# Performance work log

Measured on AMD Instinct MI355X. Metric: run time of the kernel, lower is better.

The kernel has to match this reference:

```python
import jax, jax.numpy as jnp
import numpy as np

DEGREE = 8
D = 512
K = 256
O = 512
N = 65536


def setup_inputs() -> dict:
    key = jax.random.key(0)
    ks = jax.random.split(key, 4)
    z = jax.random.normal(ks[0], (N, D), dtype=jnp.float32)
    T0 = jnp.ones((K,), dtype=jnp.float32)
    # T[i-1] corresponds to parameter T_i, i = 1..DEGREE, each [K, D]
    T = jax.random.normal(ks[1], (DEGREE, K, D), dtype=jnp.float32) * 0.02
    C_w = jax.random.normal(ks[2], (O, K), dtype=jnp.float32) * (1.0 / np.sqrt(K))
    C_b = jnp.zeros((O,), dtype=jnp.float32)
    return {"z": z, "T0": T0, "T": T, "C_w": C_w, "C_b": C_b}


def reference(z, T0, T, C_w, C_b):
    # z: [N, D]; T: [DEGREE, K, D]; recurrence over polynomial degree n:
    #   out_n = (z @ ((2n-1)/n * T_n).T) * out_{n-1} - (n-1)/n * out_{n-2}
    z = z.reshape(-1, D)
    out_prev2 = T0                                  # degree 0, [K] (broadcasts over N)
    out_prev1 = jnp.einsum('nd,kd->nk', z, T[0])    # degree 1, [N, K]
    for n in range(2, DEGREE + 1):
        a = (2.0 * n - 1.0) / n
        b = (n - 1.0) / n
        cur = jnp.einsum('nd,kd->nk', z, a * T[n - 1]) * out_prev1 - b * out_prev2
        out_prev2, out_prev1 = out_prev1, cur
    # layer_C applied to out_list[degree]
    return out_prev1 @ C_w.T + C_b
```

## Files before the change

### kernel.cpp

```cpp
#include <hip/hip_runtime.h>
#include <hip/hip_fp16.h>
#include <cstdint>

#define NROWS 65536
#define DIM   512
#define KDIM  256
#define ODIM  512
#define DEG   8
#define ZN    (NROWS * DIM)
#define TN    (DEG * KDIM * DIM)
#define CWN   (ODIM * KDIM)

typedef _Float16 f16x8 __attribute__((ext_vector_type(8)));
typedef float    f32x4 __attribute__((ext_vector_type(4)));


__device__ __forceinline__ void gld_lds16(const void* g, void* l) {
  __builtin_amdgcn_global_load_lds(
      (const __attribute__((address_space(1))) unsigned int*)g,
      (__attribute__((address_space(3))) unsigned int*)l, 16, 0, 0);
}

__device__ __forceinline__ unsigned pack2h(float a, float b) {
  union { _Float16 h[2]; unsigned u; } x;
  x.h[0] = (_Float16)a; x.h[1] = (_Float16)b;
  return x.u;
}

__device__ __forceinline__ int swz(int row, int chunk) {
  return (row << 7) | (((chunk + row) & 7) << 4);
}


__global__ void k_convert(const float* __restrict__ z,
                          const float* __restrict__ T,
                          const float* __restrict__ Cw,
                          _Float16* __restrict__ z16,
                          _Float16* __restrict__ Tb,
                          _Float16* __restrict__ Cwb) {
  long e = ((long)blockIdx.x * 256 + threadIdx.x) * 8;
  const float* src;
  _Float16* dst;
  float s = 1.0f;
  if (e < ZN) {
    src = z + e; dst = z16 + e;
  } else {
    long o = e - ZN;
    if (o < TN) {
      int n = (int)(o >> 17);
      s = (n == 0) ? 1.0f : (float)(2 * n + 1) / (float)(n + 1);
      src = T + o; dst = Tb + o;
    } else {
      long c = o - TN;
      if (c >= CWN) return;
      src = Cw + c; dst = Cwb + c;
    }
  }
  float4 v0 = *(const float4*)src;
  float4 v1 = *(const float4*)(src + 4);
  uint4 p;
  p.x = pack2h(v0.x * s, v0.y * s); p.y = pack2h(v0.z * s, v0.w * s);
  p.z = pack2h(v1.x * s, v1.y * s); p.w = pack2h(v1.z * s, v1.w * s);
  *(uint4*)dst = p;
}


__launch_bounds__(256, 3)
__global__ void k_poly(const _Float16* __restrict__ z16,
                       const float* __restrict__ T0,
                       const _Float16* __restrict__ Tb,
                       _Float16* __restrict__ u8) {
  __shared__ __align__(16) uint16_t As[128 * 64];
  __shared__ __align__(16) uint16_t Bs[2][128 * 64];

  const int tid = threadIdx.x;
  const int wave = tid >> 6, lane = tid & 63;

  const int id = blockIdx.x;
  const int super = id >> 8, rem = id & 255;
  const int kg = rem >> 4;
  const int rt = (super << 4) | (rem & 15);
  const int r0 = rt << 7;
  const int k0 = kg << 4;

  const int m_l = lane & 15, kq = lane >> 4;
  const int wrow = wave << 5;

  f32x4 acc[DEG][2];
#pragma unroll
  for (int n = 0; n < DEG; n++)
#pragma unroll
    for (int a = 0; a < 2; a++)
      acc[n][a] = (f32x4){0.f, 0.f, 0.f, 0.f};

  const _Float16* aptr[4];
  const _Float16* bptr[4];
  int lofs[4];
#pragma unroll
  for (int j = 0; j < 4; j++) {
    int lin = (j << 8) + tid;
    int row = lin >> 3;
    int c = ((lin & 7) - row) & 7;
    lofs[j] = lin << 4;
    aptr[j] = z16 + (size_t)(r0 + row) * DIM + (c << 3);
    int n = row >> 4, kk = row & 15;
    bptr[j] = Tb + (size_t)((n << 8) + k0 + kk) * DIM + (c << 3);
  }

  uint4 aR[2][4];

#pragma unroll
  for (int j = 0; j < 4; j++)
    aR[0][j] = *reinterpret_cast<const uint4*>(aptr[j]);
  __builtin_amdgcn_sched_barrier(0);
#pragma unroll
  for (int j = 0; j < 4; j++) gld_lds16(bptr[j], (char*)Bs[0] + lofs[j]);
  __builtin_amdgcn_sched_barrier(0);
#pragma unroll
  for (int j = 0; j < 4; j++)
    aR[1][j] = *reinterpret_cast<const uint4*>(aptr[j] + 64);
  __builtin_amdgcn_sched_barrier(0);

#pragma unroll
  for (int it = 0; it < DIM / 64; it++) {
    const int cur = it & 1;
    __builtin_amdgcn_s_barrier();
    if (it < DIM / 64 - 1)
      asm volatile("s_waitcnt vmcnt(4)" ::: "memory");
    else
      asm volatile("s_waitcnt vmcnt(0)" ::: "memory");
    __builtin_amdgcn_sched_barrier(0);

#pragma unroll
    for (int j = 0; j < 4; j++)
      *(uint4*)((char*)As + lofs[j]) = aR[cur][j];
    __builtin_amdgcn_sched_barrier(0);

    if (it + 1 < DIM / 64) {
#pragma unroll
      for (int j = 0; j < 4; j++)
        gld_lds16(bptr[j] + ((it + 1) << 6), (char*)Bs[cur ^ 1] + lofs[j]);
    }
    __builtin_amdgcn_sched_barrier(0);

    if (it + 2 < DIM / 64) {
#pragma unroll
      for (int j = 0; j < 4; j++)
        aR[cur][j] = *reinterpret_cast<const uint4*>(aptr[j] + ((it + 2) << 6));
    }
    __builtin_amdgcn_sched_barrier(0);

    asm volatile("s_waitcnt lgkmcnt(0)" ::: "memory");
    __builtin_amdgcn_sched_barrier(0);
    __builtin_amdgcn_s_barrier();
    __builtin_amdgcn_sched_barrier(0);

#pragma unroll
    for (int ks = 0; ks < 2; ks++) {
      const int chunk = (ks << 2) + kq;
      f16x8 af[2];
#pragma unroll
      for (int mf = 0; mf < 2; mf++)
        af[mf] = *(const f16x8*)((char*)As + swz(wrow + (mf << 4) + m_l, chunk));
#pragma unroll
      for (int n = 0; n < DEG; n++) {
        f16x8 bv = *(const f16x8*)((char*)Bs[cur] + swz((n << 4) + m_l, chunk));
#pragma unroll
        for (int mf = 0; mf < 2; mf++)
          acc[n][mf] = __builtin_amdgcn_mfma_f32_16x16x32_f16(
              af[mf], bv, acc[n][mf], 0, 0, 0);
      }
    }
  }

  const float bcoef[7] = {1.f/2.f, 2.f/3.f, 3.f/4.f, 4.f/5.f,
                          5.f/6.f, 6.f/7.f, 7.f/8.f};
  const int col = k0 + m_l;
  const float t0v = T0[col];
#pragma unroll
  for (int mf = 0; mf < 2; mf++) {
    f32x4 up2 = {t0v, t0v, t0v, t0v};
    f32x4 up1 = acc[0][mf];
#pragma unroll
    for (int n = 2; n <= DEG; n++) {
      f32x4 cur = acc[n - 1][mf] * up1 - bcoef[n - 2] * up2;
      up2 = up1; up1 = cur;
    }
    const int rbase = r0 + wrow + (mf << 4) + (kq << 2);
#pragma unroll
    for (int r = 0; r < 4; r++)
      u8[(size_t)(rbase + r) * KDIM + col] = (_Float16)up1[r];
  }
}


__launch_bounds__(256, 3)
__global__ void k_out(const _Float16* __restrict__ u8,
                      const _Float16* __restrict__ Cwb,
                      const float* __restrict__ Cb,
                      float* __restrict__ out) {
  __shared__ __align__(16) uint16_t As[2][128 * 64];
  __shared__ __align__(16) uint16_t Bs[2][64 * 64];

  const int tid = threadIdx.x;
  const int wave = tid >> 6, lane = tid & 63;

  const int id = blockIdx.x;
  const int xcd = id & 7;
  const int s = id >> 3;
  const int cg = s & 7;
  const int rt = (xcd << 6) | (s >> 3);
  const int r0 = rt << 7;
  const int c0 = cg << 6;

  const int m_l = lane & 15, kq = lane >> 4;
  const int wrow = wave << 5;

  f32x4 acc[2][4];
#pragma unroll
  for (int a = 0; a < 2; a++)
#pragma unroll
    for (int b = 0; b < 4; b++)
      acc[a][b] = (f32x4){0.f, 0.f, 0.f, 0.f};

  const _Float16* aptr[4];
  const _Float16* bptr[2];
  int lofsA[4], lofsB[2];
#pragma unroll
  for (int j = 0; j < 4; j++) {
    int lin = (j << 8) + tid;
    int row = lin >> 3;
    int c = ((lin & 7) - row) & 7;
    lofsA[j] = lin << 4;
    aptr[j] = u8 + (size_t)(r0 + row) * KDIM + (c << 3);
  }
#pragma unroll
  for (int j = 0; j < 2; j++) {
    int lin = (j << 8) + tid;
    int row = lin >> 3;
    int c = ((lin & 7) - row) & 7;
    lofsB[j] = lin << 4;
    bptr[j] = Cwb + (size_t)(c0 + row) * KDIM + (c << 3);
  }

#pragma unroll
  for (int j = 0; j < 4; j++) gld_lds16(aptr[j], (char*)As[0] + lofsA[j]);
  __builtin_amdgcn_sched_barrier(0);
#pragma unroll
  for (int j = 0; j < 2; j++) gld_lds16(bptr[j], (char*)Bs[0] + lofsB[j]);
  __builtin_amdgcn_sched_barrier(0);

#pragma unroll
  for (int it = 0; it < KDIM / 64; it++) {
    const int cur = it & 1;
    __builtin_amdgcn_s_barrier();
    __builtin_amdgcn_sched_barrier(0);

    if (it + 1 < KDIM / 64) {
#pragma unroll
      for (int j = 0; j < 4; j++)
        gld_lds16(aptr[j] + ((it + 1) << 6), (char*)As[cur ^ 1] + lofsA[j]);
      __builtin_amdgcn_sched_barrier(0);
#pragma unroll
      for (int j = 0; j < 2; j++)
        gld_lds16(bptr[j] + ((it + 1) << 6), (char*)Bs[cur ^ 1] + lofsB[j]);
      __builtin_amdgcn_sched_barrier(0);
      asm volatile("s_waitcnt vmcnt(6)" ::: "memory");
    } else {
      asm volatile("s_waitcnt vmcnt(0)" ::: "memory");
    }
    __builtin_amdgcn_sched_barrier(0);
    __builtin_amdgcn_s_barrier();
    __builtin_amdgcn_sched_barrier(0);

#pragma unroll
    for (int ks = 0; ks < 2; ks++) {
      const int chunk = (ks << 2) + kq;
      f16x8 af[2];
#pragma unroll
      for (int mf = 0; mf < 2; mf++)
        af[mf] = *(const f16x8*)((char*)As[cur] + swz(wrow + (mf << 4) + m_l, chunk));
#pragma unroll
      for (int kf = 0; kf < 4; kf++) {
        f16x8 bv = *(const f16x8*)((char*)Bs[cur] + swz((kf << 4) + m_l, chunk));
#pragma unroll
        for (int mf = 0; mf < 2; mf++)
          acc[mf][kf] = __builtin_amdgcn_mfma_f32_16x16x32_f16(
              af[mf], bv, acc[mf][kf], 0, 0, 0);
      }
    }
  }

#pragma unroll
  for (int kf = 0; kf < 4; kf++) {
    const int col = c0 + (kf << 4) + m_l;
    const float cb = Cb[col];
#pragma unroll
    for (int mf = 0; mf < 2; mf++) {
      const int rbase = r0 + wrow + (mf << 4) + (kq << 2);
#pragma unroll
      for (int r = 0; r < 4; r++)
        out[(size_t)(rbase + r) * ODIM + col] = acc[mf][kf][r] + cb;
    }
  }
}


extern "C" void kernel_launch(void* const* d_in, const int* in_sizes, int n_in,
                              void* d_out, int out_size, void* d_ws, size_t ws_size,
                              hipStream_t stream) {
  const float* z  = (const float*)d_in[0];
  const float* T0 = (const float*)d_in[1];
  const float* T  = (const float*)d_in[2];
  const float* Cw = (const float*)d_in[3];
  const float* Cb = (const float*)d_in[4];
  float* out = (float*)d_out;

  char* ws = (char*)d_ws;
  _Float16* z16 = (_Float16*)ws;
  _Float16* Tb  = (_Float16*)(ws + (size_t)ZN * 2);
  _Float16* Cwb = (_Float16*)(ws + (size_t)ZN * 2 + (size_t)TN * 2);
  _Float16* u8  = (_Float16*)(ws + (size_t)ZN * 2 + (size_t)TN * 2 + (size_t)CWN * 2);

  k_convert<<<16960, 256, 0, stream>>>(z, T, Cw, z16, Tb, Cwb);
  k_poly<<<8192, 256, 0, stream>>>(z16, T0, Tb, u8);
  k_out<<<4096, 256, 0, stream>>>(u8, Cwb, Cb, out);
}
```

Measured before the change: 394.3 us.

## Double row tiles to 256 in poly and output GEMMs, reload A via LDS-direct

Both GEMM kernels now cover 256 rows per block instead of 128, and k_out also widens to 128 output columns, so each B (T or C_w) tile is reused across twice as many rows and the grids shrink. The A operand now goes straight to single-buffered LDS through global_load_lds each iteration, replacing the register-staged double buffer in k_poly and the double-buffered A in k_out. Block-to-XCD mapping is reworked, and launch bounds drop to 2 blocks per CU to fit the larger accumulators. The cost is higher register pressure, lower occupancy, and A loads that are no longer prefetched ahead of the barrier, so load latency is more exposed.

```diff
diff --git a/kernel.cpp b/kernel.cpp
--- a/kernel.cpp
+++ b/kernel.cpp
@@ -65,92 +65,81 @@
 }
 
 
-__launch_bounds__(256, 3)
+__launch_bounds__(256, 2)
 __global__ void k_poly(const _Float16* __restrict__ z16,
                        const float* __restrict__ T0,
                        const _Float16* __restrict__ Tb,
                        _Float16* __restrict__ u8) {
-  __shared__ __align__(16) uint16_t As[128 * 64];
+  __shared__ __align__(16) uint16_t As[256 * 64];
   __shared__ __align__(16) uint16_t Bs[2][128 * 64];
 
   const int tid = threadIdx.x;
   const int wave = tid >> 6, lane = tid & 63;
 
   const int id = blockIdx.x;
-  const int super = id >> 8, rem = id & 255;
-  const int kg = rem >> 4;
-  const int rt = (super << 4) | (rem & 15);
-  const int r0 = rt << 7;
+  const int xcd = id & 7;
+  const int s = id >> 3;
+  const int kg = s & 15;
+  const int rt = (xcd << 5) | (s >> 4);
+  const int r0 = rt << 8;
   const int k0 = kg << 4;
 
   const int m_l = lane & 15, kq = lane >> 4;
-  const int wrow = wave << 5;
-
-  f32x4 acc[DEG][2];
+  const int wrow = wave << 6;
+
+  f32x4 acc[DEG][4];
 #pragma unroll
   for (int n = 0; n < DEG; n++)
 #pragma unroll
-    for (int a = 0; a < 2; a++)
+    for (int a = 0; a < 4; a++)
       acc[n][a] = (f32x4){0.f, 0.f, 0.f, 0.f};
 
-  const _Float16* aptr[4];
+  const _Float16* aptr[8];
+  int lofsA[8];
+#pragma unroll
+  for (int j = 0; j < 8; j++) {
+    int lin = (j << 8) + tid;
+    int row = lin >> 3;
+    int c = ((lin & 7) - row) & 7;
+    lofsA[j] = lin << 4;
+    aptr[j] = z16 + (size_t)(r0 + row) * DIM + (c << 3);
+  }
   const _Float16* bptr[4];
-  int lofs[4];
+  int lofsB[4];
 #pragma unroll
   for (int j = 0; j < 4; j++) {
     int lin = (j << 8) + tid;
     int row = lin >> 3;
     int c = ((lin & 7) - row) & 7;
-    lofs[j] = lin << 4;
-    aptr[j] = z16 + (size_t)(r0 + row) * DIM + (c << 3);
+    lofsB[j] = lin << 4;
     int n = row >> 4, kk = row & 15;
     bptr[j] = Tb + (size_t)((n << 8) + k0 + kk) * DIM + (c << 3);
   }
 
-  uint4 aR[2][4];
-
-#pragma unroll
-  for (int j = 0; j < 4; j++)
-    aR[0][j] = *reinterpret_cast<const uint4*>(aptr[j]);
-  __builtin_amdgcn_sched_barrier(0);
-#pragma unroll
-  for (int j = 0; j < 4; j++) gld_lds16(bptr[j], (char*)Bs[0] + lofs[j]);
-  __builtin_amdgcn_sched_barrier(0);
-#pragma unroll
-  for (int j = 0; j < 4; j++)
-    aR[1][j] = *reinterpret_cast<const uint4*>(aptr[j] + 64);
+#pragma unroll
+  for (int j = 0; j < 4; j++) gld_lds16(bptr[j], (char*)Bs[0] + lofsB[j]);
   __builtin_amdgcn_sched_barrier(0);
 
 #pragma unroll
   for (int it = 0; it < DIM / 64; it++) {
     const int cur = it & 1;
     __builtin_amdgcn_s_barrier();
-    if (it < DIM / 64 - 1)
+    __builtin_amdgcn_sched_barrier(0);
+
+#pragma unroll
+    for (int j = 0; j < 8; j++)
+      gld_lds16(aptr[j] + (it << 6), (char*)As + lofsA[j]);
+    __builtin_amdgcn_sched_barrier(0);
+
+    if (it + 1 < DIM / 64) {
+#pragma unroll
+      for (int j = 0; j < 4; j++)
+        gld_lds16(bptr[j] + ((it + 1) << 6), (char*)Bs[cur ^ 1] + lofsB[j]);
+      __builtin_amdgcn_sched_barrier(0);
       asm volatile("s_waitcnt vmcnt(4)" ::: "memory");
-    else
+    } else {
       asm volatile("s_waitcnt vmcnt(0)" ::: "memory");
-    __builtin_amdgcn_sched_barrier(0);
-
-#pragma unroll
-    for (int j = 0; j < 4; j++)
-      *(uint4*)((char*)As + lofs[j]) = aR[cur][j];
-    __builtin_amdgcn_sched_barrier(0);
-
-    if (it + 1 < DIM / 64) {
-#pragma unroll
-      for (int j = 0; j < 4; j++)
-        gld_lds16(bptr[j] + ((it + 1) << 6), (char*)Bs[cur ^ 1] + lofs[j]);
-    }
-    __builtin_amdgcn_sched_barrier(0);
-
-    if (it + 2 < DIM / 64) {
-#pragma unroll
-      for (int j = 0; j < 4; j++)
-        aR[cur][j] = *reinterpret_cast<const uint4*>(aptr[j] + ((it + 2) << 6));
-    }
-    __builtin_amdgcn_sched_barrier(0);
-
-    asm volatile("s_waitcnt lgkmcnt(0)" ::: "memory");
+    }
     __builtin_amdgcn_sched_barrier(0);
     __builtin_amdgcn_s_barrier();
     __builtin_amdgcn_sched_barrier(0);
@@ -158,15 +147,15 @@
 #pragma unroll
     for (int ks = 0; ks < 2; ks++) {
       const int chunk = (ks << 2) + kq;
-      f16x8 af[2];
-#pragma unroll
-      for (int mf = 0; mf < 2; mf++)
+      f16x8 af[4];
+#pragma unroll
+      for (int mf = 0; mf < 4; mf++)
         af[mf] = *(const f16x8*)((char*)As + swz(wrow + (mf << 4) + m_l, chunk));
 #pragma unroll
       for (int n = 0; n < DEG; n++) {
         f16x8 bv = *(const f16x8*)((char*)Bs[cur] + swz((n << 4) + m_l, chunk));
 #pragma unroll
-        for (int mf = 0; mf < 2; mf++)
+        for (int mf = 0; mf < 4; mf++)
           acc[n][mf] = __builtin_amdgcn_mfma_f32_16x16x32_f16(
               af[mf], bv, acc[n][mf], 0, 0, 0);
       }
@@ -178,7 +167,7 @@
   const int col = k0 + m_l;
   const float t0v = T0[col];
 #pragma unroll
-  for (int mf = 0; mf < 2; mf++) {
+  for (int mf = 0; mf < 4; mf++) {
     f32x4 up2 = {t0v, t0v, t0v, t0v};
     f32x4 up1 = acc[0][mf];
 #pragma unroll
@@ -194,13 +183,13 @@
 }
 
 
-__launch_bounds__(256, 3)
+__launch_bounds__(256, 2)
 __global__ void k_out(const _Float16* __restrict__ u8,
                       const _Float16* __restrict__ Cwb,
                       const float* __restrict__ Cb,
                       float* __restrict__ out) {
-  __shared__ __align__(16) uint16_t As[2][128 * 64];
-  __shared__ __align__(16) uint16_t Bs[2][64 * 64];
+  __shared__ __align__(16) uint16_t As[256 * 64];
+  __shared__ __align__(16) uint16_t Bs[2][128 * 64];
 
   const int tid = threadIdx.x;
   const int wave = tid >> 6, lane = tid & 63;
@@ -208,34 +197,35 @@
   const int id = blockIdx.x;
   const int xcd = id & 7;
   const int s = id >> 3;
-  const int cg = s & 7;
-  const int rt = (xcd << 6) | (s >> 3);
-  const int r0 = rt << 7;
-  const int c0 = cg << 6;
+  const int cg = s & 3;
+  const int rt = (xcd << 5) | (s >> 2);
+  const int r0 = rt << 8;
+  const int c0 = cg << 7;
 
   const int m_l = lane & 15, kq = lane >> 4;
-  const int wrow = wave << 5;
-
-  f32x4 acc[2][4];
-#pragma unroll
-  for (int a = 0; a < 2; a++)
-#pragma unroll
-    for (int b = 0; b < 4; b++)
+  const int wrow = wave << 6;
+
+  f32x4 acc[4][8];
+#pragma unroll
+  for (int a = 0; a < 4; a++)
+#pragma unroll
+    for (int b = 0; b < 8; b++)
       acc[a][b] = (f32x4){0.f, 0.f, 0.f, 0.f};
 
-  const _Float16* aptr[4];
-  const _Float16* bptr[2];
-  int lofsA[4], lofsB[2];
-#pragma unroll
-  for (int j = 0; j < 4; j++) {
+  const _Float16* aptr[8];
+  int lofsA[8];
+#pragma unroll
+  for (int j = 0; j < 8; j++) {
     int lin = (j << 8) + tid;
     int row = lin >> 3;
     int c = ((lin & 7) - row) & 7;
     lofsA[j] = lin << 4;
     aptr[j] = u8 + (size_t)(r0 + row) * KDIM + (c << 3);
   }
-#pragma unroll
-  for (int j = 0; j < 2; j++) {
+  const _Float16* bptr[4];
+  int lofsB[4];
+#pragma unroll
+  for (int j = 0; j < 4; j++) {
     int lin = (j << 8) + tid;
     int row = lin >> 3;
     int c = ((lin & 7) - row) & 7;
@@ -244,10 +234,7 @@
   }
 
 #pragma unroll
-  for (int j = 0; j < 4; j++) gld_lds16(aptr[j], (char*)As[0] + lofsA[j]);
-  __builtin_amdgcn_sched_barrier(0);
-#pragma unroll
-  for (int j = 0; j < 2; j++) gld_lds16(bptr[j], (char*)Bs[0] + lofsB[j]);
+  for (int j = 0; j < 4; j++) gld_lds16(bptr[j], (char*)Bs[0] + lofsB[j]);
   __builtin_amdgcn_sched_barrier(0);
 
 #pragma unroll
@@ -256,16 +243,17 @@
     __builtin_amdgcn_s_barrier();
     __builtin_amdgcn_sched_barrier(0);
 
+#pragma unroll
+    for (int j = 0; j < 8; j++)
+      gld_lds16(aptr[j] + (it << 6), (char*)As + lofsA[j]);
+    __builtin_amdgcn_sched_barrier(0);
+
     if (it + 1 < KDIM / 64) {
 #pragma unroll
       for (int j = 0; j < 4; j++)
-        gld_lds16(aptr[j] + ((it + 1) << 6), (char*)As[cur ^ 1] + lofsA[j]);
-      __builtin_amdgcn_sched_barrier(0);
-#pragma unroll
-      for (int j = 0; j < 2; j++)
         gld_lds16(bptr[j] + ((it + 1) << 6), (char*)Bs[cur ^ 1] + lofsB[j]);
       __builtin_amdgcn_sched_barrier(0);
-      asm volatile("s_waitcnt vmcnt(6)" ::: "memory");
+      asm volatile("s_waitcnt vmcnt(4)" ::: "memory");
     } else {
       asm volatile("s_waitcnt vmcnt(0)" ::: "memory");
     }
@@ -276,15 +264,15 @@
 #pragma unroll
     for (int ks = 0; ks < 2; ks++) {
       const int chunk = (ks << 2) + kq;
-      f16x8 af[2];
-#pragma unroll
-      for (int mf = 0; mf < 2; mf++)
-        af[mf] = *(const f16x8*)((char*)As[cur] + swz(wrow + (mf << 4) + m_l, chunk));
-#pragma unroll
-      for (int kf = 0; kf < 4; kf++) {
+      f16x8 af[4];
+#pragma unroll
+      for (int mf = 0; mf < 4; mf++)
+        af[mf] = *(const f16x8*)((char*)As + swz(wrow + (mf << 4) + m_l, chunk));
+#pragma unroll
+      for (int kf = 0; kf < 8; kf++) {
         f16x8 bv = *(const f16x8*)((char*)Bs[cur] + swz((kf << 4) + m_l, chunk));
 #pragma unroll
-        for (int mf = 0; mf < 2; mf++)
+        for (int mf = 0; mf < 4; mf++)
           acc[mf][kf] = __builtin_amdgcn_mfma_f32_16x16x32_f16(
               af[mf], bv, acc[mf][kf], 0, 0, 0);
       }
@@ -292,11 +280,11 @@
   }
 
 #pragma unroll
-  for (int kf = 0; kf < 4; kf++) {
+  for (int kf = 0; kf < 8; kf++) {
     const int col = c0 + (kf << 4) + m_l;
     const float cb = Cb[col];
 #pragma unroll
-    for (int mf = 0; mf < 2; mf++) {
+    for (int mf = 0; mf < 4; mf++) {
       const int rbase = r0 + wrow + (mf << 4) + (kq << 2);
 #pragma unroll
       for (int r = 0; r < 4; r++)
@@ -323,6 +311,6 @@
   _Float16* u8  = (_Float16*)(ws + (size_t)ZN * 2 + (size_t)TN * 2 + (size_t)CWN * 2);
 
   k_convert<<<16960, 256, 0, stream>>>(z, T, Cw, z16, Tb, Cwb);
-  k_poly<<<8192, 256, 0, stream>>>(z16, T0, Tb, u8);
-  k_out<<<4096, 256, 0, stream>>>(u8, Cwb, Cb, out);
-}
+  k_poly<<<4096, 256, 0, stream>>>(z16, T0, Tb, u8);
+  k_out<<<1024, 256, 0, stream>>>(u8, Cwb, Cb, out);
+}
```

Measured after the change: 393.1 us. No clear change (-0.3%).

## Enlarge k_poly row tile to 256 with direct-to-LDS double-buffered A loads

Applied to the files above, without the earlier changes.

Doubles the k_poly row tile from 128 to 256 rows per block, so each wave computes 64 rows and the T tile is reused across twice as many rows. The K step shrinks to 32, and both z and T now go straight to LDS through global_load_lds with double buffering, replacing register staging of z. Block IDs are remapped so each XCD handles a contiguous set of row tiles, and MFMA sections are wrapped in s_setprio. The cost is more accumulator registers (occupancy bound drops to 2 blocks) and twice as many loop iterations with barriers.

```diff
diff --git a/kernel.cpp b/kernel.cpp
--- a/kernel.cpp
+++ b/kernel.cpp
@@ -29,6 +29,10 @@
 
 __device__ __forceinline__ int swz(int row, int chunk) {
   return (row << 7) | (((chunk + row) & 7) << 4);
+}
+
+__device__ __forceinline__ int swz32(int row, int chunk) {
+  return (row << 6) | (((chunk + row + (row >> 2)) & 3) << 4);
 }
 
 
@@ -65,112 +69,100 @@
 }
 
 
-__launch_bounds__(256, 3)
+__launch_bounds__(256, 2)
 __global__ void k_poly(const _Float16* __restrict__ z16,
                        const float* __restrict__ T0,
                        const _Float16* __restrict__ Tb,
                        _Float16* __restrict__ u8) {
-  __shared__ __align__(16) uint16_t As[128 * 64];
-  __shared__ __align__(16) uint16_t Bs[2][128 * 64];
+  __shared__ __align__(16) uint16_t As[2][256 * 32];
+  __shared__ __align__(16) uint16_t Bs[2][128 * 32];
 
   const int tid = threadIdx.x;
   const int wave = tid >> 6, lane = tid & 63;
 
   const int id = blockIdx.x;
-  const int super = id >> 8, rem = id & 255;
-  const int kg = rem >> 4;
-  const int rt = (super << 4) | (rem & 15);
-  const int r0 = rt << 7;
+  const int xcd = id & 7;
+  const int s = id >> 3;
+  const int kg = s & 15;
+  const int rt = (xcd << 5) | (s >> 4);
+  const int r0 = rt << 8;
   const int k0 = kg << 4;
 
   const int m_l = lane & 15, kq = lane >> 4;
-  const int wrow = wave << 5;
-
-  f32x4 acc[DEG][2];
+  const int wrow = wave << 6;
+
+  f32x4 acc[DEG][4];
 #pragma unroll
   for (int n = 0; n < DEG; n++)
 #pragma unroll
-    for (int a = 0; a < 2; a++)
+    for (int a = 0; a < 4; a++)
       acc[n][a] = (f32x4){0.f, 0.f, 0.f, 0.f};
 
   const _Float16* aptr[4];
-  const _Float16* bptr[4];
-  int lofs[4];
+  int lofsA[4];
 #pragma unroll
   for (int j = 0; j < 4; j++) {
     int lin = (j << 8) + tid;
-    int row = lin >> 3;
-    int c = ((lin & 7) - row) & 7;
-    lofs[j] = lin << 4;
+    int row = lin >> 2;
+    int c = ((lin & 3) - row - (row >> 2)) & 3;
+    lofsA[j] = lin << 4;
     aptr[j] = z16 + (size_t)(r0 + row) * DIM + (c << 3);
+  }
+  const _Float16* bptr[2];
+  int lofsB[2];
+#pragma unroll
+  for (int j = 0; j < 2; j++) {
+    int lin = (j << 8) + tid;
+    int row = lin >> 2;
+    int c = ((lin & 3) - row - (row >> 2)) & 3;
+    lofsB[j] = lin << 4;
     int n = row >> 4, kk = row & 15;
     bptr[j] = Tb + (size_t)((n << 8) + k0 + kk) * DIM + (c << 3);
   }
 
-  uint4 aR[2][4];
-
-#pragma unroll
-  for (int j = 0; j < 4; j++)
-    aR[0][j] = *reinterpret_cast<const uint4*>(aptr[j]);
+#pragma unroll
+  for (int j = 0; j < 4; j++) gld_lds16(aptr[j], (char*)As[0] + lofsA[j]);
+#pragma unroll
+  for (int j = 0; j < 2; j++) gld_lds16(bptr[j], (char*)Bs[0] + lofsB[j]);
   __builtin_amdgcn_sched_barrier(0);
-#pragma unroll
-  for (int j = 0; j < 4; j++) gld_lds16(bptr[j], (char*)Bs[0] + lofs[j]);
-  __builtin_amdgcn_sched_barrier(0);
-#pragma unroll
-  for (int j = 0; j < 4; j++)
-    aR[1][j] = *reinterpret_cast<const uint4*>(aptr[j] + 64);
-  __builtin_amdgcn_sched_barrier(0);
-
-#pragma unroll
-  for (int it = 0; it < DIM / 64; it++) {
+
+#pragma unroll
+  for (int it = 0; it < DIM / 32; it++) {
     const int cur = it & 1;
     __builtin_amdgcn_s_barrier();
-    if (it < DIM / 64 - 1)
-      asm volatile("s_waitcnt vmcnt(4)" ::: "memory");
-    else
+    __builtin_amdgcn_sched_barrier(0);
+
+    if (it + 1 < DIM / 32) {
+#pragma unroll
+      for (int j = 0; j < 4; j++)
+        gld_lds16(aptr[j] + ((it + 1) << 5), (char*)As[cur ^ 1] + lofsA[j]);
+#pragma unroll
+      for (int j = 0; j < 2; j++)
+        gld_lds16(bptr[j] + ((it + 1) << 5), (char*)Bs[cur ^ 1] + lofsB[j]);
+      __builtin_amdgcn_sched_barrier(0);
+      asm volatile("s_waitcnt vmcnt(6)" ::: "memory");
+    } else {
       asm volatile("s_waitcnt vmcnt(0)" ::: "memory");
-    __builtin_amdgcn_sched_barrier(0);
-
-#pragma unroll
-    for (int j = 0; j < 4; j++)
-      *(uint4*)((char*)As + lofs[j]) = aR[cur][j];
-    __builtin_amdgcn_sched_barrier(0);
-
-    if (it + 1 < DIM / 64) {
-#pragma unroll
-      for (int j = 0; j < 4; j++)
-        gld_lds16(bptr[j] + ((it + 1) << 6), (char*)Bs[cur ^ 1] + lofs[j]);
-    }
-    __builtin_amdgcn_sched_barrier(0);
-
-    if (it + 2 < DIM / 64) {
-#pragma unroll
-      for (int j = 0; j < 4; j++)
-        aR[cur][j] = *reinterpret_cast<const uint4*>(aptr[j] + ((it + 2) << 6));
-    }
-    __builtin_amdgcn_sched_barrier(0);
-
-    asm volatile("s_waitcnt lgkmcnt(0)" ::: "memory");
+    }
     __builtin_amdgcn_sched_barrier(0);
     __builtin_amdgcn_s_barrier();
     __builtin_amdgcn_sched_barrier(0);
 
-#pragma unroll
-    for (int ks = 0; ks < 2; ks++) {
-      const int chunk = (ks << 2) + kq;
-      f16x8 af[2];
-#pragma unroll
-      for (int mf = 0; mf < 2; mf++)
-        af[mf] = *(const f16x8*)((char*)As + swz(wrow + (mf << 4) + m_l, chunk));
-#pragma unroll
-      for (int n = 0; n < DEG; n++) {
-        f16x8 bv = *(const f16x8*)((char*)Bs[cur] + swz((n << 4) + m_l, chunk));
-#pragma unroll
-        for (int mf = 0; mf < 2; mf++)
-          acc[n][mf] = __builtin_amdgcn_mfma_f32_16x16x32_f16(
-              af[mf], bv, acc[n][mf], 0, 0, 0);
-      }
-    }
+    f16x8 af[4];
+#pragma unroll
+    for (int mf = 0; mf < 4; mf++)
+      af[mf] = *(const f16x8*)((char*)As[cur] +
+                               swz32(wrow + (mf << 4) + m_l, kq));
+    __builtin_amdgcn_s_setprio(1);
+#pragma unroll
+    for (int n = 0; n < DEG; n++) {
+      f16x8 bv = *(const f16x8*)((char*)Bs[cur] + swz32((n << 4) + m_l, kq));
+#pragma unroll
+      for (int mf = 0; mf < 4; mf++)
+        acc[n][mf] = __builtin_amdgcn_mfma_f32_16x16x32_f16(
+            af[mf], bv, acc[n][mf], 0, 0, 0);
+    }
+    __builtin_amdgcn_s_setprio(0);
   }
 
   const float bcoef[7] = {1.f/2.f, 2.f/3.f, 3.f/4.f, 4.f/5.f,
@@ -178,7 +170,7 @@
   const int col = k0 + m_l;
   const float t0v = T0[col];
 #pragma unroll
-  for (int mf = 0; mf < 2; mf++) {
+  for (int mf = 0; mf < 4; mf++) {
     f32x4 up2 = {t0v, t0v, t0v, t0v};
     f32x4 up1 = acc[0][mf];
 #pragma unroll
@@ -323,6 +315,6 @@
   _Float16* u8  = (_Float16*)(ws + (size_t)ZN * 2 + (size_t)TN * 2 + (size_t)CWN * 2);
 
   k_convert<<<16960, 256, 0, stream>>>(z, T, Cw, z16, Tb, Cwb);
-  k_poly<<<8192, 256, 0, stream>>>(z16, T0, Tb, u8);
+  k_poly<<<4096, 256, 0, stream>>>(z16, T0, Tb, u8);
   k_out<<<4096, 256, 0, stream>>>(u8, Cwb, Cb, out);
 }
```

After: 392.4 us. No clear change (-0.5%).
